# Optimization experiments

Measured on AMD Instinct MI355X. Metric: run time of the kernel, lower is better.

The kernel has to match this reference:

```python
import jax, jax.numpy as jnp
import numpy as np

B, N, H, IN, OUT = 2, 4096, 64, 32, 8


def setup_inputs() -> dict:
    key = jax.random.key(0)
    ks = jax.random.split(key, 18)
    sc = 0.1  # xavier-ish scale for H=64
    mask = lambda k: (jax.random.uniform(k, (1, N, N)) < 0.1).astype(jnp.float32)
    return {
        "x0": jax.random.normal(ks[0], (B, N, IN), jnp.float32),
        "h0": jax.random.normal(ks[1], (B, N, H), jnp.float32),
        "h1": jax.random.normal(ks[2], (B, N, H), jnp.float32),
        "h2": jax.random.normal(ks[3], (B, N, H), jnp.float32),
        "m00": mask(ks[4]), "m20": mask(ks[5]), "m01": mask(ks[6]),
        "m11": mask(ks[7]), "m12": mask(ks[8]), "m22": mask(ks[9]),
        "Wq": jax.random.normal(ks[10], (3, H, H), jnp.float32) * sc,
        "Wk": jax.random.normal(ks[11], (6, H, H), jnp.float32) * sc,
        "Wsu0": jax.random.normal(ks[12], (H, IN + H), jnp.float32) * sc,
        "Wsu12": jax.random.normal(ks[13], (2, H, H), jnp.float32) * sc,
        "Wdt": jax.random.normal(ks[14], (3, H, H), jnp.float32) * sc,
        "bdt": jnp.zeros((3, H), jnp.float32),
        "step_size": jnp.array(1.0, jnp.float32),
        "out_scale": jnp.array(10.0, jnp.float32),
    }


def _cosine_acc(q, keys_and_masks_and_vals):
    # q: [B,N,H]; each entry: (keys [B,Np,H], mask [1,N,Np], vals [B,Np,H])
    qn = q / jnp.linalg.norm(q, axis=2, keepdims=True)
    acc = 0.0
    for k, m, v in keys_and_masks_and_vals:
        kn = k / jnp.linalg.norm(k, axis=2, keepdims=True)
        scale = 1.0 / jnp.sum(m, axis=2, keepdims=True)
        rel = scale * m * jnp.einsum("bnh,bmh->bnm", qn, kn)  # [B,N,Np]
        acc = acc + jnp.einsum("bnm,bmh->bnh", rel, v)
    return acc


def reference(x0, h0, h1, h2, m00, m20, m01, m11, m12, m22,
              Wq, Wk, Wsu0, Wsu12, Wdt, bdt, step_size, out_scale):
    # queries per successor type, keys per edge; edges (pred->succ):
    # 0->0 (k0), 2->0 (k1), 0->1 (k2), 1->1 (k3), 1->2 (k4), 2->2 (k5)
    q0 = h0 @ Wq[0].T
    q1 = h1 @ Wq[1].T
    q2 = h2 @ Wq[2].T
    acc0 = _cosine_acc(q0, [(h0 @ Wk[0].T, m00, h0), (h2 @ Wk[1].T, m20, h2)])
    acc1 = _cosine_acc(q1, [(h0 @ Wk[2].T, m01, h0), (h1 @ Wk[3].T, m11, h1)])
    acc2 = _cosine_acc(q2, [(h1 @ Wk[4].T, m12, h1), (h2 @ Wk[5].T, m22, h2)])

    def step(h, acc_in, Wsu, t):
        dt = 2.0 * jax.nn.sigmoid(h @ Wdt[t].T + bdt[t]) - 1.0
        return h + step_size * dt * (acc_in @ Wsu.T)

    h0n = step(h0, jnp.concatenate([x0, acc0], axis=2), Wsu0, 0)
    h1n = step(h1, acc1, Wsu12[0], 1)
    h2n = step(h2, acc2, Wsu12[1], 2)
    out2 = out_scale * h2n[:, :, :OUT]
    return (out2, h0n, h1n, h2n)
```

## Files before the change

### kernel.cpp

```cpp
#include <hip/hip_runtime.h>

typedef __bf16 bf16;
typedef bf16 bf16x8 __attribute__((ext_vector_type(8)));
typedef float f32x4 __attribute__((ext_vector_type(4)));
typedef unsigned int uint;
typedef uint u32x2 __attribute__((ext_vector_type(2)));
typedef uint u32x4 __attribute__((ext_vector_type(4)));
typedef unsigned short u16x8 __attribute__((ext_vector_type(8)));

constexpr int NT = 4096;

__device__ __forceinline__ bf16x8 ld8f(const float* p) {
    f32x4 a = *(const f32x4*)p;
    f32x4 b = *(const f32x4*)(p + 4);
    bf16x8 v;
    v[0] = (bf16)a[0]; v[1] = (bf16)a[1]; v[2] = (bf16)a[2]; v[3] = (bf16)a[3];
    v[4] = (bf16)b[0]; v[5] = (bf16)b[1]; v[6] = (bf16)b[2]; v[7] = (bf16)b[3];
    return v;
}

__device__ __forceinline__ uint pack2(float a, float b) {
    unsigned short ua = __builtin_bit_cast(unsigned short, (bf16)a);
    unsigned short ub = __builtin_bit_cast(unsigned short, (bf16)b);
    return (uint)ua | ((uint)ub << 16);
}

__global__ __launch_bounds__(256) void mask_kernel(
    const float* __restrict__ m00, const float* __restrict__ m20, const float* __restrict__ m01,
    const float* __restrict__ m11, const float* __restrict__ m12, const float* __restrict__ m22,
    uint* __restrict__ mb, float* __restrict__ rs2)
{
    const int tid = threadIdx.x, wid = tid >> 6, lane = tid & 63;
    const int mi = blockIdx.x;
    const int e = mi >> 10, rb = mi & 1023;
    const int row = rb * 4 + wid;
    const float* masks[6] = {m00, m20, m01, m11, m12, m22};
    const float* mrow = masks[e] + (size_t)row * NT;
    const int own_it = lane >> 2;
    const uint s = (uint)(lane & 3) * 16;

    f32x4 buf[4];
#pragma unroll
    for (int p = 0; p < 4; p++)
        buf[p] = *(const f32x4*)(mrow + 256 * p + 4 * lane);

    uint lo = 0, hi = 0, cnt = 0;
#pragma unroll
    for (int it = 0; it < 16; it++) {
        f32x4 v = buf[it & 3];
        if (it + 4 < 16)
            buf[it & 3] = *(const f32x4*)(mrow + 256 * (it + 4) + 4 * lane);
        unsigned long long b0 = __ballot(v[0] > 0.5f);
        unsigned long long b1 = __ballot(v[1] > 0.5f);
        unsigned long long b2 = __ballot(v[2] > 0.5f);
        unsigned long long b3 = __ballot(v[3] > 0.5f);
        cnt += __popcll(b0) + __popcll(b1) + __popcll(b2) + __popcll(b3);
        uint locand = ((uint)(b0 >> s) & 0xFFFFu) | (((uint)(b1 >> s) & 0xFFFFu) << 16);
        uint hicand = ((uint)(b2 >> s) & 0xFFFFu) | (((uint)(b3 >> s) & 0xFFFFu) << 16);
        if (own_it == it) { lo = locand; hi = hicand; }
    }
    if (lane == 0) rs2[e * NT + row] = (float)cnt;
    u32x2 w = {lo, hi};
    ((u32x2*)(mb + (size_t)(e * NT + row) * 128))[lane] = w;
}

__global__ __launch_bounds__(256) void prep_kernel(
    const float* __restrict__ h0, const float* __restrict__ h1, const float* __restrict__ h2,
    const float* __restrict__ Wq, const float* __restrict__ Wk,
    bf16* __restrict__ qn, bf16* __restrict__ kn, bf16* __restrict__ vT)
{
    __shared__ __align__(16) unsigned short tlds[4][16][72];
    const int tid = threadIdx.x, wid = tid >> 6, lane = tid & 63;
    const int l15 = lane & 15, quad = lane >> 4;
    const int bx = blockIdx.x;
    const int rt = bx & 127, sl = bx >> 7;
    const int g0 = rt * 64;
    const int grow = g0 + wid * 16 + l15;
    const float* hs[3] = {h0, h1, h2};
    const int predmap[6] = {0, 2, 0, 1, 1, 2};

    if (sl >= 9) {
        const int p = sl - 9;
        bf16x8 af[2];
#pragma unroll
        for (int hc = 0; hc < 2; hc++)
            af[hc] = ld8f(hs[p] + (size_t)grow * 64 + hc * 32 + quad * 8);
#pragma unroll
        for (int hc = 0; hc < 2; hc++)
            *(u16x8*)(&tlds[wid][l15][hc * 32 + quad * 8]) = __builtin_bit_cast(u16x8, af[hc]);
        unsigned short vals[16];
#pragma unroll
        for (int r = 0; r < 16; r++) vals[r] = tlds[wid][r][lane];
        uint us[8];
#pragma unroll
        for (int k = 0; k < 8; k++) us[k] = (uint)vals[2 * k] | ((uint)vals[2 * k + 1] << 16);
        const int gr0 = g0 + wid * 16;
        const int bb = gr0 >> 12, n0 = gr0 & 4095;
        uint* dst = (uint*)(vT + ((size_t)(p * 2 + bb) * 64 + lane) * NT + n0);
        u32x4 w0 = {us[0], us[1], us[2], us[3]};
        u32x4 w1 = {us[4], us[5], us[6], us[7]};
        *(u32x4*)dst = w0;
        *(u32x4*)(dst + 4) = w1;
        return;
    }

    const int pj = sl;
    const float* W = (pj < 3) ? (Wq + pj * 4096) : (Wk + (pj - 3) * 4096);
    const int src = (pj < 3) ? pj : predmap[pj - 3];
    bf16* outp = (pj < 3) ? (qn + (size_t)pj * 2 * NT * 64)
                          : (kn + (size_t)(pj - 3) * 2 * NT * 64);
    bf16x8 af[2];
#pragma unroll
    for (int hc = 0; hc < 2; hc++)
        af[hc] = ld8f(hs[src] + (size_t)grow * 64 + hc * 32 + quad * 8);

    f32x4 s[4];
#pragma unroll
    for (int it = 0; it < 4; it++) {
        f32x4 acc = {0.f, 0.f, 0.f, 0.f};
#pragma unroll
        for (int hc = 0; hc < 2; hc++) {
            bf16x8 wb = ld8f(W + (size_t)(it * 16 + l15) * 64 + hc * 32 + quad * 8);
            acc = __builtin_amdgcn_mfma_f32_16x16x32_bf16(af[hc], wb, acc, 0, 0, 0);
        }
        s[it] = acc;
    }
#pragma unroll
    for (int r = 0; r < 4; r++) {
        float ss = s[0][r] * s[0][r] + s[1][r] * s[1][r] + s[2][r] * s[2][r] + s[3][r] * s[3][r];
        ss += __shfl_xor(ss, 1); ss += __shfl_xor(ss, 2);
        ss += __shfl_xor(ss, 4); ss += __shfl_xor(ss, 8);
        float rn = rsqrtf(ss);
        s[0][r] *= rn; s[1][r] *= rn; s[2][r] *= rn; s[3][r] *= rn;
    }
    const int rowbase = g0 + wid * 16 + quad * 4;
#pragma unroll
    for (int it = 0; it < 4; it++)
#pragma unroll
        for (int r = 0; r < 4; r++)
            outp[(size_t)(rowbase + r) * 64 + it * 16 + l15] = (bf16)s[it][r];
}

template<int JC>
__global__ __launch_bounds__(256, 4) void attn_kernel(
    const bf16* __restrict__ qn, const bf16* __restrict__ kn, const bf16* __restrict__ vT,
    const uint* __restrict__ mb, float* __restrict__ Pacc)
{
    __shared__ __align__(16) bf16 Klds[2][64][72];
    __shared__ __align__(16) bf16 Vlds[2][64][72];
    const int tid = threadIdx.x, wid = tid >> 6, lane = tid & 63;
    const int l15 = lane & 15, quad = lane >> 4;
    constexpr int G = 6 * 32 * 2 * JC;
    const int bxr = blockIdx.x;
    const int wg = (bxr & 7) * (G >> 3) + (bxr >> 3);
    const int jcv = wg % JC;
    int r = wg / JC;
    const int b = r & 1; r >>= 1;
    const int qt = r & 31; const int e = r >> 5;
    const int qtypemap[6] = {0, 0, 1, 1, 2, 2};
    const int predmap[6]  = {0, 2, 0, 1, 1, 2};
    const int qtv = qtypemap[e], pv = predmap[e];
    const int qrow0 = qt * 128, wstrip = wid * 32;
    constexpr int JSPAN = NT / JC;
    constexpr int NI = JSPAN / 64;
    const int jbeg = jcv * JSPAN;

    int srow[2], sch[2];
#pragma unroll
    for (int s = 0; s < 2; s++) {
        int u = tid + 256 * s;
        srow[s] = u >> 3; sch[s] = u & 7;
    }
    const bf16* Ksrc = kn + ((size_t)(e * 2 + b) * NT + jbeg) * 64;
    const bf16* Vsrc = vT + (size_t)(pv * 2 + b) * 64 * NT + jbeg;

    bf16x8 Qf[2][2];
#pragma unroll
    for (int mt = 0; mt < 2; mt++)
#pragma unroll
        for (int hc = 0; hc < 2; hc++)
            Qf[mt][hc] = *(const bf16x8*)(qn +
                ((size_t)(qtv * 2 + b) * NT + qrow0 + wstrip + mt * 16 + l15) * 64 +
                hc * 32 + quad * 8);

    f32x4 acc2[4][2];
#pragma unroll
    for (int ht = 0; ht < 4; ht++)
#pragma unroll
        for (int mt = 0; mt < 2; mt++) {
            f32x4 z = {0.f, 0.f, 0.f, 0.f};
            acc2[ht][mt] = z;
        }

    const uint* mbase[2];
#pragma unroll
    for (int mt = 0; mt < 2; mt++)
        mbase[mt] = mb + (size_t)(e * NT + qrow0 + wstrip + mt * 16 + l15) * 128 + (jbeg >> 5);

    u32x4 kreg[2], vreg[2];
#pragma unroll
    for (int s = 0; s < 2; s++) {
        kreg[s] = *(const u32x4*)(Ksrc + (size_t)srow[s] * 64 + sch[s] * 8);
        vreg[s] = *(const u32x4*)(Vsrc + (size_t)srow[s] * NT + sch[s] * 8);
    }
    u32x2 mcur[2], mnxt[2];
#pragma unroll
    for (int mt = 0; mt < 2; mt++) {
        mcur[mt] = *(const u32x2*)(mbase[mt]);
        mnxt[mt] = *(const u32x2*)(mbase[mt] + ((NI > 1) ? 2 : 0));
    }
#pragma unroll
    for (int s = 0; s < 2; s++) {
        *(u32x4*)(&Klds[0][srow[s]][sch[s] * 8]) = kreg[s];
        *(u32x4*)(&Vlds[0][srow[s]][sch[s] * 8]) = vreg[s];
    }
    {
        const int j1 = (NI > 1) ? 64 : 0;
#pragma unroll
        for (int s = 0; s < 2; s++) {
            kreg[s] = *(const u32x4*)(Ksrc + (size_t)(j1 + srow[s]) * 64 + sch[s] * 8);
            vreg[s] = *(const u32x4*)(Vsrc + (size_t)srow[s] * NT + j1 + sch[s] * 8);
        }
    }
    __syncthreads();

#pragma unroll 1
    for (int ji = 0; ji < NI; ji++) {
        const int cur = ji & 1;
        const int woff2 = (ji + 2 < NI) ? 2 * (ji + 2) : 0;
        u32x2 mtmp[2];
#pragma unroll
        for (int mt = 0; mt < 2; mt++)
            mtmp[mt] = *(const u32x2*)(mbase[mt] + woff2);

        uint Pd[4][2][2];
#pragma unroll
        for (int jt = 0; jt < 4; jt++) {
            bf16x8 aK0 = *(const bf16x8*)(&Klds[cur][jt * 16 + l15][quad * 8]);
            bf16x8 aK1 = *(const bf16x8*)(&Klds[cur][jt * 16 + l15][32 + quad * 8]);
#pragma unroll
            for (int mt = 0; mt < 2; mt++) {
                f32x4 sc = {0.f, 0.f, 0.f, 0.f};
                sc = __builtin_amdgcn_mfma_f32_16x16x32_bf16(aK0, Qf[mt][0], sc, 0, 0, 0);
                sc = __builtin_amdgcn_mfma_f32_16x16x32_bf16(aK1, Qf[mt][1], sc, 0, 0, 0);
#pragma unroll
                for (int k = 0; k < 4; k++) {
                    const uint w = (k < 2) ? mcur[mt].x : mcur[mt].y;
                    sc[k] = ((w >> ((k & 1) * 16 + jt * 4 + quad)) & 1u) ? sc[k] : 0.0f;
                }
                Pd[jt][mt][0] = pack2(sc[0], sc[1]);
                Pd[jt][mt][1] = pack2(sc[2], sc[3]);
            }
        }
#pragma unroll
        for (int mt = 0; mt < 2; mt++) { mcur[mt] = mnxt[mt]; mnxt[mt] = mtmp[mt]; }

        uint Bf[2][2][4];
#pragma unroll
        for (int mt = 0; mt < 2; mt++)
#pragma unroll
            for (int c = 0; c < 2; c++)
#pragma unroll
                for (int d = 0; d < 2; d++) {
                    uint x = Pd[2 * c][mt][d];
                    uint y = Pd[2 * c + 1][mt][d];
                    asm("v_permlane32_swap_b32 %0, %1\n\t"
                        "v_permlane16_swap_b32 %0, %1"
                        : "+v"(x), "+v"(y));
                    Bf[mt][c][d]     = x;
                    Bf[mt][c][d + 2] = y;
                }

#pragma unroll
        for (int ht = 0; ht < 4; ht++)
#pragma unroll
            for (int c = 0; c < 2; c++) {
                bf16x8 a = *(const bf16x8*)(&Vlds[cur][ht * 16 + l15][c * 32 + quad * 8]);
#pragma unroll
                for (int mt = 0; mt < 2; mt++) {
                    u32x4 t = {Bf[mt][c][0], Bf[mt][c][1], Bf[mt][c][2], Bf[mt][c][3]};
                    bf16x8 bbv = __builtin_bit_cast(bf16x8, t);
                    acc2[ht][mt] =
                        __builtin_amdgcn_mfma_f32_16x16x32_bf16(a, bbv, acc2[ht][mt], 0, 0, 0);
                }
            }

        if (ji + 1 < NI) {
            const int nxt = cur ^ 1;
#pragma unroll
            for (int s = 0; s < 2; s++) {
                *(u32x4*)(&Klds[nxt][srow[s]][sch[s] * 8]) = kreg[s];
                *(u32x4*)(&Vlds[nxt][srow[s]][sch[s] * 8]) = vreg[s];
            }
            const int j2 = (ji + 2 < NI) ? (ji + 2) * 64 : 0;
#pragma unroll
            for (int s = 0; s < 2; s++) {
                kreg[s] = *(const u32x4*)(Ksrc + (size_t)(j2 + srow[s]) * 64 + sch[s] * 8);
                vreg[s] = *(const u32x4*)(Vsrc + (size_t)srow[s] * NT + j2 + sch[s] * 8);
            }
            __syncthreads();
        }
    }

#pragma unroll
    for (int ht = 0; ht < 4; ht++)
#pragma unroll
        for (int mt = 0; mt < 2; mt++) {
            const int n = qrow0 + wstrip + mt * 16 + l15;
            *(f32x4*)(Pacc + ((((size_t)(jcv * 6 + e) * 2 + b) * NT + n) << 6) +
                      ht * 16 + quad * 4) = acc2[ht][mt];
        }
}

template<int JC>
__global__ __launch_bounds__(256) void update_kernel(
    const float* __restrict__ x0, const float* __restrict__ h0,
    const float* __restrict__ h1, const float* __restrict__ h2,
    const float* __restrict__ Wsu0, const float* __restrict__ Wsu12,
    const float* __restrict__ Wdt, const float* __restrict__ bdt,
    const float* __restrict__ stepp, const float* __restrict__ oscp,
    const float* __restrict__ Pacc, const float* __restrict__ rs2,
    float* __restrict__ dout)
{
    const int tid = threadIdx.x, wid = tid >> 6, lane = tid & 63;
    const int l15 = lane & 15, quad = lane >> 4;
    const int bx = blockIdx.x;
    const int ih = (bx >= 384) ? 1 : 0;
    const int base = bx - ih * 384;
    const int rt = base & 127, t = base >> 7;
    const int g0 = rt * 64;
    const int grow = g0 + wid * 16 + l15;
    const int n = grow & 4095, bb = grow >> 12;
    const float step = *stepp, osc = *oscp;
    const float* hs[3] = {h0, h1, h2};
    const float* __restrict__ ht_base = hs[t];

    bf16x8 afh[2], afacc[2], afx;
#pragma unroll
    for (int hc = 0; hc < 2; hc++)
        afh[hc] = ld8f(ht_base + (size_t)grow * 64 + hc * 32 + quad * 8);
    if (t == 0) afx = ld8f(x0 + (size_t)grow * 32 + quad * 8);

    const float i0 = 1.f / rs2[(size_t)(2 * t) * NT + n];
    const float i1 = 1.f / rs2[(size_t)(2 * t + 1) * NT + n];
#pragma unroll
    for (int hc = 0; hc < 2; hc++) {
        f32x4 S0a = {0.f,0.f,0.f,0.f}, S0b = {0.f,0.f,0.f,0.f};
        f32x4 S1a = {0.f,0.f,0.f,0.f}, S1b = {0.f,0.f,0.f,0.f};
#pragma unroll
        for (int jc = 0; jc < JC; jc++) {
            const float* p0 = Pacc + ((((size_t)(jc * 6 + 2 * t) * 2 + bb) * NT + n) << 6) +
                              hc * 32 + quad * 8;
            const float* p1 = Pacc + ((((size_t)(jc * 6 + 2 * t + 1) * 2 + bb) * NT + n) << 6) +
                              hc * 32 + quad * 8;
            S0a += *(const f32x4*)p0;  S0b += *(const f32x4*)(p0 + 4);
            S1a += *(const f32x4*)p1;  S1b += *(const f32x4*)(p1 + 4);
        }
        bf16x8 v;
#pragma unroll
        for (int j = 0; j < 4; j++) v[j]     = (bf16)(S0a[j] * i0 + S1a[j] * i1);
#pragma unroll
        for (int j = 0; j < 4; j++) v[4 + j] = (bf16)(S0b[j] * i0 + S1b[j] * i1);
        afacc[hc] = v;
    }

#pragma unroll
    for (int ii = 0; ii < 2; ii++) {
        const int it = ih * 2 + ii;
        const float bdtv = bdt[t * 64 + it * 16 + l15];
        f32x4 z = {0.f, 0.f, 0.f, 0.f};
        f32x4 u = {0.f, 0.f, 0.f, 0.f};
#pragma unroll
        for (int hc = 0; hc < 2; hc++) {
            bf16x8 wb = ld8f(Wdt + (size_t)t * 4096 + (size_t)(it * 16 + l15) * 64 + hc * 32 + quad * 8);
            z = __builtin_amdgcn_mfma_f32_16x16x32_bf16(afh[hc], wb, z, 0, 0, 0);
        }
        if (t == 0) {
            bf16x8 w0 = ld8f(Wsu0 + (size_t)(it * 16 + l15) * 96 + quad * 8);
            u = __builtin_amdgcn_mfma_f32_16x16x32_bf16(afx, w0, u, 0, 0, 0);
#pragma unroll
            for (int kc = 0; kc < 2; kc++) {
                bf16x8 wk = ld8f(Wsu0 + (size_t)(it * 16 + l15) * 96 + 32 + kc * 32 + quad * 8);
                u = __builtin_amdgcn_mfma_f32_16x16x32_bf16(afacc[kc], wk, u, 0, 0, 0);
            }
        } else {
#pragma unroll
            for (int kc = 0; kc < 2; kc++) {
                bf16x8 wk = ld8f(Wsu12 + (size_t)(t - 1) * 4096 + (size_t)(it * 16 + l15) * 64 + kc * 32 + quad * 8);
                u = __builtin_amdgcn_mfma_f32_16x16x32_bf16(afacc[kc], wk, u, 0, 0, 0);
            }
        }
        const int colg = it * 16 + l15;
#pragma unroll
        for (int r = 0; r < 4; r++) {
            int row = g0 + wid * 16 + quad * 4 + r;
            float zz = z[r] + bdtv;
            float dtv = 2.f / (1.f + __expf(-zz)) - 1.f;
            float hval = ht_base[(size_t)row * 64 + colg];
            float hn = hval + step * dtv * u[r];
            dout[65536 + (size_t)t * 524288 + (size_t)row * 64 + colg] = hn;
            if (t == 2 && colg < 8)
                dout[(size_t)row * 8 + colg] = osc * hn;
        }
    }
}

extern "C" void kernel_launch(void* const* d_in, const int* in_sizes, int n_in,
                              void* d_out, int out_size, void* d_ws, size_t ws_size,
                              hipStream_t stream) {
    const float* x0   = (const float*)d_in[0];
    const float* h0   = (const float*)d_in[1];
    const float* h1   = (const float*)d_in[2];
    const float* h2   = (const float*)d_in[3];
    const float* m00  = (const float*)d_in[4];
    const float* m20  = (const float*)d_in[5];
    const float* m01  = (const float*)d_in[6];
    const float* m11  = (const float*)d_in[7];
    const float* m12  = (const float*)d_in[8];
    const float* m22  = (const float*)d_in[9];
    const float* Wq   = (const float*)d_in[10];
    const float* Wk   = (const float*)d_in[11];
    const float* Wsu0 = (const float*)d_in[12];
    const float* Wsu12= (const float*)d_in[13];
    const float* Wdt  = (const float*)d_in[14];
    const float* bdt  = (const float*)d_in[15];
    const float* step = (const float*)d_in[16];
    const float* oscl = (const float*)d_in[17];

    bf16* qn  = (bf16*)d_ws;
    bf16* kn  = qn + 1572864;
    bf16* vT  = kn + 3145728;
    uint* mb  = (uint*)(vT + 1572864);
    float* rs2 = (float*)(mb + 3145728);
    float* Pacc = rs2 + 24576;

    auto need = [](size_t jc) { return 25264128 + jc * 12582912; };
    const int JC = (ws_size >= need(4)) ? 4 : ((ws_size >= need(2)) ? 2 : 1);

    mask_kernel<<<6144, 256, 0, stream>>>(m00, m20, m01, m11, m12, m22, mb, rs2);
    prep_kernel<<<1536, 256, 0, stream>>>(h0, h1, h2, Wq, Wk, qn, kn, vT);

    if (JC == 4) {
        attn_kernel<4><<<6 * 32 * 2 * 4, 256, 0, stream>>>(qn, kn, vT, mb, Pacc);
        update_kernel<4><<<768, 256, 0, stream>>>(x0, h0, h1, h2, Wsu0, Wsu12, Wdt, bdt,
                                                  step, oscl, Pacc, rs2, (float*)d_out);
    } else if (JC == 2) {
        attn_kernel<2><<<6 * 32 * 2 * 2, 256, 0, stream>>>(qn, kn, vT, mb, Pacc);
        update_kernel<2><<<768, 256, 0, stream>>>(x0, h0, h1, h2, Wsu0, Wsu12, Wdt, bdt,
                                                  step, oscl, Pacc, rs2, (float*)d_out);
    } else {
        attn_kernel<1><<<6 * 32 * 2 * 1, 256, 0, stream>>>(qn, kn, vT, mb, Pacc);
        update_kernel<1><<<768, 256, 0, stream>>>(x0, h0, h1, h2, Wsu0, Wsu12, Wdt, bdt,
                                                  step, oscl, Pacc, rs2, (float*)d_out);
    }
}
```

Before: 482.1 us.

## Store attention partial sums in bf16 and widen mask kernel load batching

The attention kernel now writes its per-chunk partial accumulators as bf16 instead of fp32, and the update kernel reads bf16x8 vectors and sums them in fp32. This halves the intermediate Pacc traffic and the workspace it needs, so a larger JC fits. Separately, the mask kernel processes two 256-column slabs per iteration, keeping eight loads in flight and halving loop trips. Rounding partial sums to bf16 adds error before the cross-chunk reduction.

```diff
diff --git a/kernel.cpp b/kernel.cpp
--- a/kernel.cpp
+++ b/kernel.cpp
@@ -6,6 +6,7 @@
 typedef unsigned int uint;
 typedef uint u32x2 __attribute__((ext_vector_type(2)));
 typedef uint u32x4 __attribute__((ext_vector_type(4)));
+typedef unsigned short u16x4 __attribute__((ext_vector_type(4)));
 typedef unsigned short u16x8 __attribute__((ext_vector_type(8)));
 
 constexpr int NT = 4096;
@@ -36,28 +37,42 @@
     const int row = rb * 4 + wid;
     const float* masks[6] = {m00, m20, m01, m11, m12, m22};
     const float* mrow = masks[e] + (size_t)row * NT;
-    const int own_it = lane >> 2;
-    const uint s = (uint)(lane & 3) * 16;
-
-    f32x4 buf[4];
-#pragma unroll
-    for (int p = 0; p < 4; p++)
-        buf[p] = *(const f32x4*)(mrow + 256 * p + 4 * lane);
+    const int own_it = lane >> 3;
+    const int q = lane & 7;
+    const uint s = (uint)(q & 3) * 16;
+
+    f32x4 bufA[4], bufB[4];
+#pragma unroll
+    for (int p = 0; p < 4; p++) {
+        bufA[p] = *(const f32x4*)(mrow + 512 * p + 4 * lane);
+        bufB[p] = *(const f32x4*)(mrow + 512 * p + 256 + 4 * lane);
+    }
 
     uint lo = 0, hi = 0, cnt = 0;
 #pragma unroll
-    for (int it = 0; it < 16; it++) {
-        f32x4 v = buf[it & 3];
-        if (it + 4 < 16)
-            buf[it & 3] = *(const f32x4*)(mrow + 256 * (it + 4) + 4 * lane);
-        unsigned long long b0 = __ballot(v[0] > 0.5f);
-        unsigned long long b1 = __ballot(v[1] > 0.5f);
-        unsigned long long b2 = __ballot(v[2] > 0.5f);
-        unsigned long long b3 = __ballot(v[3] > 0.5f);
-        cnt += __popcll(b0) + __popcll(b1) + __popcll(b2) + __popcll(b3);
-        uint locand = ((uint)(b0 >> s) & 0xFFFFu) | (((uint)(b1 >> s) & 0xFFFFu) << 16);
-        uint hicand = ((uint)(b2 >> s) & 0xFFFFu) | (((uint)(b3 >> s) & 0xFFFFu) << 16);
-        if (own_it == it) { lo = locand; hi = hicand; }
+    for (int it = 0; it < 8; it++) {
+        f32x4 vA = bufA[it & 3], vB = bufB[it & 3];
+        if (it + 4 < 8) {
+            bufA[it & 3] = *(const f32x4*)(mrow + 512 * (it + 4) + 4 * lane);
+            bufB[it & 3] = *(const f32x4*)(mrow + 512 * (it + 4) + 256 + 4 * lane);
+        }
+        unsigned long long a0 = __ballot(vA[0] > 0.5f);
+        unsigned long long a1 = __ballot(vA[1] > 0.5f);
+        unsigned long long a2 = __ballot(vA[2] > 0.5f);
+        unsigned long long a3 = __ballot(vA[3] > 0.5f);
+        unsigned long long b0 = __ballot(vB[0] > 0.5f);
+        unsigned long long b1 = __ballot(vB[1] > 0.5f);
+        unsigned long long b2 = __ballot(vB[2] > 0.5f);
+        unsigned long long b3 = __ballot(vB[3] > 0.5f);
+        cnt += __popcll(a0) + __popcll(a1) + __popcll(a2) + __popcll(a3)
+             + __popcll(b0) + __popcll(b1) + __popcll(b2) + __popcll(b3);
+        uint loA = ((uint)(a0 >> s) & 0xFFFFu) | (((uint)(a1 >> s) & 0xFFFFu) << 16);
+        uint hiA = ((uint)(a2 >> s) & 0xFFFFu) | (((uint)(a3 >> s) & 0xFFFFu) << 16);
+        uint loB = ((uint)(b0 >> s) & 0xFFFFu) | (((uint)(b1 >> s) & 0xFFFFu) << 16);
+        uint hiB = ((uint)(b2 >> s) & 0xFFFFu) | (((uint)(b3 >> s) & 0xFFFFu) << 16);
+        uint lox = (q < 4) ? loA : loB;
+        uint hix = (q < 4) ? hiA : hiB;
+        if (own_it == it) { lo = lox; hi = hix; }
     }
     if (lane == 0) rs2[e * NT + row] = (float)cnt;
     u32x2 w = {lo, hi};
@@ -144,7 +159,7 @@
 template<int JC>
 __global__ __launch_bounds__(256, 4) void attn_kernel(
     const bf16* __restrict__ qn, const bf16* __restrict__ kn, const bf16* __restrict__ vT,
-    const uint* __restrict__ mb, float* __restrict__ Pacc)
+    const uint* __restrict__ mb, bf16* __restrict__ Pacc)
 {
     __shared__ __align__(16) bf16 Klds[2][64][72];
     __shared__ __align__(16) bf16 Vlds[2][64][72];
@@ -307,8 +322,12 @@
 #pragma unroll
         for (int mt = 0; mt < 2; mt++) {
             const int n = qrow0 + wstrip + mt * 16 + l15;
-            *(f32x4*)(Pacc + ((((size_t)(jcv * 6 + e) * 2 + b) * NT + n) << 6) +
-                      ht * 16 + quad * 4) = acc2[ht][mt];
+            u16x4 pk;
+#pragma unroll
+            for (int r2 = 0; r2 < 4; r2++)
+                pk[r2] = __builtin_bit_cast(unsigned short, (bf16)acc2[ht][mt][r2]);
+            *(u16x4*)(Pacc + ((((size_t)(jcv * 6 + e) * 2 + b) * NT + n) << 6) +
+                      ht * 16 + quad * 4) = pk;
         }
 }
 
@@ -319,7 +338,7 @@
     const float* __restrict__ Wsu0, const float* __restrict__ Wsu12,
     const float* __restrict__ Wdt, const float* __restrict__ bdt,
     const float* __restrict__ stepp, const float* __restrict__ oscp,
-    const float* __restrict__ Pacc, const float* __restrict__ rs2,
+    const bf16* __restrict__ Pacc, const float* __restrict__ rs2,
     float* __restrict__ dout)
 {
     const int tid = threadIdx.x, wid = tid >> 6, lane = tid & 63;
@@ -345,22 +364,21 @@
     const float i1 = 1.f / rs2[(size_t)(2 * t + 1) * NT + n];
 #pragma unroll
     for (int hc = 0; hc < 2; hc++) {
-        f32x4 S0a = {0.f,0.f,0.f,0.f}, S0b = {0.f,0.f,0.f,0.f};
-        f32x4 S1a = {0.f,0.f,0.f,0.f}, S1b = {0.f,0.f,0.f,0.f};
+        float S0[8] = {0,0,0,0,0,0,0,0}, S1[8] = {0,0,0,0,0,0,0,0};
 #pragma unroll
         for (int jc = 0; jc < JC; jc++) {
-            const float* p0 = Pacc + ((((size_t)(jc * 6 + 2 * t) * 2 + bb) * NT + n) << 6) +
-                              hc * 32 + quad * 8;
-            const float* p1 = Pacc + ((((size_t)(jc * 6 + 2 * t + 1) * 2 + bb) * NT + n) << 6) +
-                              hc * 32 + quad * 8;
-            S0a += *(const f32x4*)p0;  S0b += *(const f32x4*)(p0 + 4);
-            S1a += *(const f32x4*)p1;  S1b += *(const f32x4*)(p1 + 4);
+            const bf16* p0 = Pacc + ((((size_t)(jc * 6 + 2 * t) * 2 + bb) * NT + n) << 6) +
+                             hc * 32 + quad * 8;
+            const bf16* p1 = Pacc + ((((size_t)(jc * 6 + 2 * t + 1) * 2 + bb) * NT + n) << 6) +
+                             hc * 32 + quad * 8;
+            bf16x8 v0 = *(const bf16x8*)p0;
+            bf16x8 v1 = *(const bf16x8*)p1;
+#pragma unroll
+            for (int j = 0; j < 8; j++) { S0[j] += (float)v0[j]; S1[j] += (float)v1[j]; }
         }
         bf16x8 v;
 #pragma unroll
-        for (int j = 0; j < 4; j++) v[j]     = (bf16)(S0a[j] * i0 + S1a[j] * i1);
-#pragma unroll
-        for (int j = 0; j < 4; j++) v[4 + j] = (bf16)(S0b[j] * i0 + S1b[j] * i1);
+        for (int j = 0; j < 8; j++) v[j] = (bf16)(S0[j] * i0 + S1[j] * i1);
         afacc[hc] = v;
     }
 
@@ -432,9 +450,9 @@
     bf16* vT  = kn + 3145728;
     uint* mb  = (uint*)(vT + 1572864);
     float* rs2 = (float*)(mb + 3145728);
-    float* Pacc = rs2 + 24576;
-
-    auto need = [](size_t jc) { return 25264128 + jc * 12582912; };
+    bf16* Pacc = (bf16*)(rs2 + 24576);
+
+    auto need = [](size_t jc) { return 25264128 + jc * 6291456; };
     const int JC = (ws_size >= need(4)) ? 4 : ((ws_size >= need(2)) ? 2 : 1);
 
     mask_kernel<<<6144, 256, 0, stream>>>(m00, m20, m01, m11, m12, m22, mb, rs2);
```

After: 475.8 us. Within noise of the previous version (-1.3%).
